# Performance work log

Measured on AMD Instinct MI355X. Metric: run time of the kernel, lower is better.

Reference implementation:

```python
import jax, jax.numpy as jnp
import numpy as np

POS_WEIGHT = 5.0

def setup_inputs() -> dict:
    key = jax.random.key(0)
    k1, k2, k3, k4 = jax.random.split(key, 4)
    B, S, P = 128, 32768, 65536
    preds = jax.random.normal(k1, (B, S), dtype=jnp.float32)
    targets = jax.random.randint(k2, (B, S), 0, 2, dtype=jnp.int32)
    # monotone (sorted) warping-path indices, like a DTW alignment path
    pi = jnp.sort(jax.random.randint(k3, (B, P), 0, S), axis=1)
    pj = jnp.sort(jax.random.randint(k4, (B, P), 0, S), axis=1)
    paths = jnp.stack([pi, pj], axis=-1).astype(jnp.int64)  # [B, P, 2]
    return {"preds": preds, "targets": targets, "paths": paths}

def _per_batch_loss(pred, target, path):
    # pred: [S], target: [S] int, path: [P, 2] of (i, j) pairs
    S = pred.shape[0]
    P = path.shape[0]
    pi, pj = path[:, 0], path[:, 1]
    steps = jnp.arange(P)
    # first step index k at which each target position j appears in the path
    first_k = jax.ops.segment_min(steps, pj, num_segments=S)  # [S]
    is_first = steps == first_k[pj]                            # first occurrence of j
    hit = (target[pj] == 1) & is_first                         # first-match to an SoS target
    # scatter-first-write: gt[i] = 1 for the matched pred positions
    gt = jnp.zeros((S,), dtype=pred.dtype).at[pi].max(hit.astype(pred.dtype))
    # BCEWithLogitsLoss with pos_weight, mean reduction (numerically stable)
    loss = -(POS_WEIGHT * gt * jax.nn.log_sigmoid(pred)
             + (1.0 - gt) * jax.nn.log_sigmoid(-pred))
    return loss.mean()

def reference(preds, targets, paths):
    per_batch = jax.vmap(_per_batch_loss)(preds, targets, paths)  # [B]
    return per_batch.mean()  # sum over batch / batch_size
```

## Files before the change

kernel.cpp:

```cpp
#include <hip/hip_runtime.h>

#define NB 128
#define NS 32768
#define NP 65536
#define POS_W 5.0f

constexpr int MASK_WORDS = (NB * NS) / 32;
constexpr int WPB        = NS / 32;
constexpr int LOSS_BLOCKS = 1024;


__global__ __launch_bounds__(256)
void tbit_kernel(const int* __restrict__ targets, unsigned int* __restrict__ tb) {
    constexpr int NSEG = NB * NS / 64;
    const int lane = threadIdx.x & 63;
    const int wid  = (blockIdx.x * blockDim.x + threadIdx.x) >> 6;
    const int nw   = (gridDim.x * blockDim.x) >> 6;
    for (int s = wid; s < NSEG; s += nw) {
        const unsigned long long m = __ballot(targets[(size_t)s * 64 + lane] != 0);
        if (lane == 0)       tb[s * 2]     = (unsigned int)m;
        else if (lane == 32) tb[s * 2 + 1] = (unsigned int)(m >> 32);
    }
}

template <int QPB>
__global__ __launch_bounds__(512)
void gt_kernel(const int* __restrict__ pw, const unsigned int* __restrict__ tbits_g,
               unsigned int* __restrict__ pmask) {
    __shared__ unsigned int tbits[WPB];
    __shared__ unsigned int gbits[WPB];

    const int is64 = (pw[2 * (size_t)NP - 1] == 0);

    const int q   = blockIdx.x;
    const int b   = blockIdx.y;
    const int tid = threadIdx.x;

    tbits[tid]       = tbits_g[(size_t)b * WPB + tid];
    tbits[tid + 512] = tbits_g[(size_t)b * WPB + tid + 512];
    gbits[tid]       = 0u;
    gbits[tid + 512] = 0u;
    __syncthreads();

    constexpr int STEPS = NP / QPB;
    constexpr int SPT   = STEPS / 512;
    const int    k0 = q * STEPS + tid * SPT;
    const size_t s0 = (size_t)b * NP + (size_t)k0;
    const int4*  p4 = (const int4*)pw;

    int prev = -1;
    if (is64) {
        if (k0 != 0) prev = pw[4 * s0 - 2];
        #pragma unroll
        for (int c = 0; c < SPT / 16; ++c) {
            const size_t base = s0 + (size_t)c * 16;
            int4 a[16];
            #pragma unroll
            for (int j = 0; j < 16; ++j) a[j] = p4[base + j];
            #pragma unroll
            for (int j = 0; j < 16; ++j) {
                const int pi = a[j].x, pj = a[j].z;
                const bool f = (pj != prev);
                prev = pj;
                if (f && ((tbits[pj >> 5] >> (pj & 31)) & 1u))
                    atomicOr(&gbits[pi >> 5], 1u << (pi & 31));
            }
        }
    } else {
        if (k0 != 0) prev = pw[2 * s0 - 1];
        #pragma unroll
        for (int c = 0; c < SPT / 16; ++c) {
            const size_t base = (s0 >> 1) + (size_t)c * 8;
            int4 a[8];
            #pragma unroll
            for (int j = 0; j < 8; ++j) a[j] = p4[base + j];
            #pragma unroll
            for (int j = 0; j < 8; ++j) {
                {
                    const int pi = a[j].x, pj = a[j].y;
                    const bool f = (pj != prev);
                    prev = pj;
                    if (f && ((tbits[pj >> 5] >> (pj & 31)) & 1u))
                        atomicOr(&gbits[pi >> 5], 1u << (pi & 31));
                }
                {
                    const int pi = a[j].z, pj = a[j].w;
                    const bool f = (pj != prev);
                    prev = pj;
                    if (f && ((tbits[pj >> 5] >> (pj & 31)) & 1u))
                        atomicOr(&gbits[pi >> 5], 1u << (pi & 31));
                }
            }
        }
    }
    __syncthreads();

    unsigned int* dst = pmask + (size_t)q * MASK_WORDS + (size_t)b * WPB;
    dst[tid]       = gbits[tid];
    dst[tid + 512] = gbits[tid + 512];
}

template <int QPB>
__global__ __launch_bounds__(256)
void loss_kernel(const float* __restrict__ preds, const unsigned int* __restrict__ pmask,
                 float* __restrict__ partials) {
    constexpr int N4 = (NB * NS) / 4;
    float acc = 0.f;
    const int stride = gridDim.x * blockDim.x;
    for (int idx = blockIdx.x * blockDim.x + threadIdx.x; idx < N4; idx += stride) {
        const float4 x = reinterpret_cast<const float4*>(preds)[idx];
        unsigned int mw = 0u;
        #pragma unroll
        for (int q = 0; q < QPB; ++q)
            mw |= pmask[(size_t)q * MASK_WORDS + (idx >> 3)];
        const unsigned int m = mw >> ((idx & 7) * 4);
        const float xs[4] = {x.x, x.y, x.z, x.w};
#pragma unroll
        for (int j = 0; j < 4; ++j) {
            const float v = xs[j];
            const float t = __logf(1.f + __expf(-fabsf(v)));
            const float sp_pos = t + fmaxf(v, 0.f);
            const float sp_neg = sp_pos - v;
            acc += ((m >> j) & 1u) ? POS_W * sp_neg : sp_pos;
        }
    }
    for (int off = 32; off; off >>= 1) acc += __shfl_down(acc, off);
    __shared__ float sacc[4];
    const int wave = threadIdx.x >> 6, lane = threadIdx.x & 63;
    if (lane == 0) sacc[wave] = acc;
    __syncthreads();
    if (threadIdx.x == 0) {
        float s = 0.f;
#pragma unroll
        for (int w = 0; w < 4; ++w) s += sacc[w];
        partials[blockIdx.x] = s;
    }
}

__global__ __launch_bounds__(256)
void final_kernel(const float* __restrict__ partials, float* __restrict__ out) {
    float acc = 0.f;
    for (int i = threadIdx.x; i < LOSS_BLOCKS; i += 256) acc += partials[i];
    for (int off = 32; off; off >>= 1) acc += __shfl_down(acc, off);
    __shared__ float sacc[4];
    const int wave = threadIdx.x >> 6, lane = threadIdx.x & 63;
    if (lane == 0) sacc[wave] = acc;
    __syncthreads();
    if (threadIdx.x == 0) {
        float s = 0.f;
#pragma unroll
        for (int w = 0; w < 4; ++w) s += sacc[w];
        out[0] = s * (1.0f / ((float)NB * (float)NS));
    }
}

extern "C" void kernel_launch(void* const* d_in, const int* in_sizes, int n_in,
                              void* d_out, int out_size, void* d_ws, size_t ws_size,
                              hipStream_t stream) {
    const float* preds   = (const float*)d_in[0];
    const int*   targets = (const int*)d_in[1];
    const int*   paths_w = (const int*)d_in[2];
    float*       out     = (float*)d_out;

    int qpb = 8;
    while (qpb > 1 &&
           ws_size < (size_t)(1 + qpb) * MASK_WORDS * 4 + (size_t)LOSS_BLOCKS * 4)
        qpb >>= 1;

    unsigned int* tbits_g  = (unsigned int*)d_ws;
    unsigned int* pmask    = tbits_g + MASK_WORDS;
    float*        partials = (float*)((char*)d_ws +
                              (size_t)(1 + qpb) * MASK_WORDS * 4);

    tbit_kernel<<<1024, 256, 0, stream>>>(targets, tbits_g);

    dim3 g1(qpb, NB);
    switch (qpb) {
        case 8:
            gt_kernel<8><<<g1, 512, 0, stream>>>(paths_w, tbits_g, pmask);
            loss_kernel<8><<<LOSS_BLOCKS, 256, 0, stream>>>(preds, pmask, partials);
            break;
        case 4:
            gt_kernel<4><<<g1, 512, 0, stream>>>(paths_w, tbits_g, pmask);
            loss_kernel<4><<<LOSS_BLOCKS, 256, 0, stream>>>(preds, pmask, partials);
            break;
        case 2:
            gt_kernel<2><<<g1, 512, 0, stream>>>(paths_w, tbits_g, pmask);
            loss_kernel<2><<<LOSS_BLOCKS, 256, 0, stream>>>(preds, pmask, partials);
            break;
        default:
            gt_kernel<1><<<g1, 512, 0, stream>>>(paths_w, tbits_g, pmask);
            loss_kernel<1><<<LOSS_BLOCKS, 256, 0, stream>>>(preds, pmask, partials);
            break;
    }

    final_kernel<<<1, 256, 0, stream>>>(partials, out);
}
```

Baseline: 35.24 us.

## Coalesce path loads with wave shuffles and fuse final reduction via atomics

The gt kernel now has consecutive threads read consecutive path elements, so loads are coalesced instead of each thread scanning a private contiguous chunk. The previous-j value comes from a neighbour lane via __shfl_up, and lane 0 takes a preloaded boundary value. The final reduction kernel is replaced by a fixed-point 64-bit atomic accumulation with a last-block-done counter, removing one launch at the cost of a memset and atomics. QPB=1 support is dropped.

```diff
diff --git a/kernel.cpp b/kernel.cpp
--- a/kernel.cpp
+++ b/kernel.cpp
@@ -8,6 +8,7 @@
 constexpr int MASK_WORDS = (NB * NS) / 32;
 constexpr int WPB        = NS / 32;
 constexpr int LOSS_BLOCKS = 1024;
+constexpr double FXSCALE = 4294967296.0;
 
 
 __global__ __launch_bounds__(256)
@@ -32,9 +33,11 @@
 
     const int is64 = (pw[2 * (size_t)NP - 1] == 0);
 
-    const int q   = blockIdx.x;
-    const int b   = blockIdx.y;
-    const int tid = threadIdx.x;
+    const int q    = blockIdx.x;
+    const int b    = blockIdx.y;
+    const int tid  = threadIdx.x;
+    const int lane = tid & 63;
+    const int wbase = tid & ~63;
 
     tbits[tid]       = tbits_g[(size_t)b * WPB + tid];
     tbits[tid + 512] = tbits_g[(size_t)b * WPB + tid + 512];
@@ -43,53 +46,61 @@
     __syncthreads();
 
     constexpr int STEPS = NP / QPB;
-    constexpr int SPT   = STEPS / 512;
-    const int    k0 = q * STEPS + tid * SPT;
-    const size_t s0 = (size_t)b * NP + (size_t)k0;
-    const int4*  p4 = (const int4*)pw;
+    const int    k0    = q * STEPS;
+    const size_t sbase = (size_t)b * NP + k0;
+    const int4*  p4    = (const int4*)pw;
 
-    int prev = -1;
-    if (is64) {
-        if (k0 != 0) prev = pw[4 * s0 - 2];
+    if (!is64) {
+        constexpr int NIT = STEPS / 1024;
+        constexpr int NCH = (NIT + 7) / 8;
+        const size_t pb = sbase >> 1;
+        int bval = -1;
+        if (lane < NIT) {
+            const int kf = k0 + (lane * 512 + wbase) * 2;
+            if (kf != 0) bval = pw[2 * ((size_t)b * NP + kf) - 1];
+        }
         #pragma unroll
-        for (int c = 0; c < SPT / 16; ++c) {
-            const size_t base = s0 + (size_t)c * 16;
-            int4 a[16];
+        for (int ch = 0; ch < NCH; ++ch) {
+            int4 a[8];
             #pragma unroll
-            for (int j = 0; j < 16; ++j) a[j] = p4[base + j];
+            for (int j = 0; j < 8; ++j) a[j] = p4[pb + (ch * 8 + j) * 512 + tid];
             #pragma unroll
-            for (int j = 0; j < 16; ++j) {
-                const int pi = a[j].x, pj = a[j].z;
-                const bool f = (pj != prev);
-                prev = pj;
-                if (f && ((tbits[pj >> 5] >> (pj & 31)) & 1u))
-                    atomicOr(&gbits[pi >> 5], 1u << (pi & 31));
+            for (int j = 0; j < 8; ++j) {
+                const int it = ch * 8 + j;
+                const int pi0 = a[j].x, pj0 = a[j].y, pi1 = a[j].z, pj1 = a[j].w;
+                const int pl = __shfl_up(pj1, 1);
+                const int bv = __shfl(bval, it);
+                const int prev = (lane == 0) ? bv : pl;
+                const bool f0 = (pj0 != prev);
+                const bool f1 = (pj1 != pj0);
+                if (f0 && ((tbits[pj0 >> 5] >> (pj0 & 31)) & 1u))
+                    atomicOr(&gbits[pi0 >> 5], 1u << (pi0 & 31));
+                if (f1 && ((tbits[pj1 >> 5] >> (pj1 & 31)) & 1u))
+                    atomicOr(&gbits[pi1 >> 5], 1u << (pi1 & 31));
             }
         }
     } else {
-        if (k0 != 0) prev = pw[2 * s0 - 1];
+        constexpr int NIT = STEPS / 512;
+        constexpr int NCH = (NIT + 7) / 8;
+        int bval = -1;
+        if (lane < NIT) {
+            const int kf = k0 + lane * 512 + wbase;
+            if (kf != 0) bval = pw[4 * ((size_t)b * NP + kf) - 2];
+        }
         #pragma unroll
-        for (int c = 0; c < SPT / 16; ++c) {
-            const size_t base = (s0 >> 1) + (size_t)c * 8;
+        for (int ch = 0; ch < NCH; ++ch) {
             int4 a[8];
             #pragma unroll
-            for (int j = 0; j < 8; ++j) a[j] = p4[base + j];
+            for (int j = 0; j < 8; ++j) a[j] = p4[sbase + (ch * 8 + j) * 512 + tid];
             #pragma unroll
             for (int j = 0; j < 8; ++j) {
-                {
-                    const int pi = a[j].x, pj = a[j].y;
-                    const bool f = (pj != prev);
-                    prev = pj;
-                    if (f && ((tbits[pj >> 5] >> (pj & 31)) & 1u))
-                        atomicOr(&gbits[pi >> 5], 1u << (pi & 31));
-                }
-                {
-                    const int pi = a[j].z, pj = a[j].w;
-                    const bool f = (pj != prev);
-                    prev = pj;
-                    if (f && ((tbits[pj >> 5] >> (pj & 31)) & 1u))
-                        atomicOr(&gbits[pi >> 5], 1u << (pi & 31));
-                }
+                const int it = ch * 8 + j;
+                const int pi = a[j].x, pj = a[j].z;
+                const int pl = __shfl_up(pj, 1);
+                const int bv = __shfl(bval, it);
+                const int prev = (lane == 0) ? bv : pl;
+                if ((pj != prev) && ((tbits[pj >> 5] >> (pj & 31)) & 1u))
+                    atomicOr(&gbits[pi >> 5], 1u << (pi & 31));
             }
         }
     }
@@ -103,7 +114,8 @@
 template <int QPB>
 __global__ __launch_bounds__(256)
 void loss_kernel(const float* __restrict__ preds, const unsigned int* __restrict__ pmask,
-                 float* __restrict__ partials) {
+                 unsigned long long* __restrict__ acc64, unsigned int* __restrict__ cnt,
+                 float* __restrict__ out) {
     constexpr int N4 = (NB * NS) / 4;
     float acc = 0.f;
     const int stride = gridDim.x * blockDim.x;
@@ -133,24 +145,15 @@
         float s = 0.f;
 #pragma unroll
         for (int w = 0; w < 4; ++w) s += sacc[w];
-        partials[blockIdx.x] = s;
-    }
-}
-
-__global__ __launch_bounds__(256)
-void final_kernel(const float* __restrict__ partials, float* __restrict__ out) {
-    float acc = 0.f;
-    for (int i = threadIdx.x; i < LOSS_BLOCKS; i += 256) acc += partials[i];
-    for (int off = 32; off; off >>= 1) acc += __shfl_down(acc, off);
-    __shared__ float sacc[4];
-    const int wave = threadIdx.x >> 6, lane = threadIdx.x & 63;
-    if (lane == 0) sacc[wave] = acc;
-    __syncthreads();
-    if (threadIdx.x == 0) {
-        float s = 0.f;
-#pragma unroll
-        for (int w = 0; w < 4; ++w) s += sacc[w];
-        out[0] = s * (1.0f / ((float)NB * (float)NS));
+        const unsigned long long fx = (unsigned long long)((double)s * FXSCALE + 0.5);
+        atomicAdd(acc64, fx);
+        __threadfence();
+        const unsigned int c = atomicAdd(cnt, 1u);
+        if (c == (unsigned int)gridDim.x - 1u) {
+            __threadfence();
+            const unsigned long long tot = atomicAdd(acc64, 0ull);
+            out[0] = (float)((double)tot * (1.0 / FXSCALE) / ((double)NB * (double)NS));
+        }
     }
 }
 
@@ -163,36 +166,32 @@
     float*       out     = (float*)d_out;
 
     int qpb = 8;
-    while (qpb > 1 &&
-           ws_size < (size_t)(1 + qpb) * MASK_WORDS * 4 + (size_t)LOSS_BLOCKS * 4)
+    while (qpb > 2 &&
+           ws_size < (size_t)(1 + qpb) * MASK_WORDS * 4 + 16)
         qpb >>= 1;
 
-    unsigned int* tbits_g  = (unsigned int*)d_ws;
-    unsigned int* pmask    = tbits_g + MASK_WORDS;
-    float*        partials = (float*)((char*)d_ws +
-                              (size_t)(1 + qpb) * MASK_WORDS * 4);
+    unsigned int*        tbits_g = (unsigned int*)d_ws;
+    unsigned int*        pmask   = tbits_g + MASK_WORDS;
+    char*                tail    = (char*)d_ws + (size_t)(1 + qpb) * MASK_WORDS * 4;
+    unsigned long long*  acc64   = (unsigned long long*)tail;
+    unsigned int*        cnt     = (unsigned int*)(tail + 8);
 
+    hipMemsetAsync(tail, 0, 16, stream);
     tbit_kernel<<<1024, 256, 0, stream>>>(targets, tbits_g);
 
     dim3 g1(qpb, NB);
     switch (qpb) {
         case 8:
             gt_kernel<8><<<g1, 512, 0, stream>>>(paths_w, tbits_g, pmask);
-            loss_kernel<8><<<LOSS_BLOCKS, 256, 0, stream>>>(preds, pmask, partials);
+            loss_kernel<8><<<LOSS_BLOCKS, 256, 0, stream>>>(preds, pmask, acc64, cnt, out);
             break;
         case 4:
             gt_kernel<4><<<g1, 512, 0, stream>>>(paths_w, tbits_g, pmask);
-            loss_kernel<4><<<LOSS_BLOCKS, 256, 0, stream>>>(preds, pmask, partials);
-            break;
-        case 2:
-            gt_kernel<2><<<g1, 512, 0, stream>>>(paths_w, tbits_g, pmask);
-            loss_kernel<2><<<LOSS_BLOCKS, 256, 0, stream>>>(preds, pmask, partials);
+            loss_kernel<4><<<LOSS_BLOCKS, 256, 0, stream>>>(preds, pmask, acc64, cnt, out);
             break;
         default:
-            gt_kernel<1><<<g1, 512, 0, stream>>>(paths_w, tbits_g, pmask);
-            loss_kernel<1><<<LOSS_BLOCKS, 256, 0, stream>>>(preds, pmask, partials);
+            gt_kernel<2><<<g1, 512, 0, stream>>>(paths_w, tbits_g, pmask);
+            loss_kernel<2><<<LOSS_BLOCKS, 256, 0, stream>>>(preds, pmask, acc64, cnt, out);
             break;
     }
-
-    final_kernel<<<1, 256, 0, stream>>>(partials, out);
 }
```

Measured after the change: 63.82 us. +81.1%, slower.
